# Optimization experiments

Measured on AMD Instinct MI355X. Metric: run time of the kernel, lower is better.

The kernel has to match this reference:

```python
import jax, jax.numpy as jnp
from jax import lax
import numpy as np

B, NQ, NT = 32, 256, 512
INF = jnp.float32(1e30)  # stand-in for float('inf') mask fill; all targets are valid here
W_TRANS, W_QPOS, W_ROT = 1.0, 1.0, 1.0


def setup_inputs() -> dict:
    key = jax.random.key(0)
    k1, k2, k3, k4 = jax.random.split(key, 4)
    rot = jax.random.normal(k3, (B, NQ, 4), jnp.float32)
    rot = rot / jnp.linalg.norm(rot, axis=-1, keepdims=True)  # unit quaternions
    return {
        "translation_norm": jax.random.normal(k1, (B, NQ, 3), jnp.float32),
        "qpos_norm": jax.random.normal(k2, (B, NQ, 16), jnp.float32),
        "rotation": rot,
        "norm_pose": jax.random.normal(k4, (B, NT, 23), jnp.float32),
    }


def _l1_cost(p, t):
    # p: [B, NQ, D], t: [B, NT, D] -> [B, NQ, NT] pairwise L1
    return jnp.abs(p[:, :, None, :] - t[:, None, :, :]).sum(-1)


def _final_cost(translation_norm, qpos_norm, rotation, norm_pose):
    valid = jnp.abs(norm_pose).sum(-1) > 0  # [B, NT]
    cost = (W_TRANS * _l1_cost(translation_norm, norm_pose[..., :3])
            + W_QPOS * _l1_cost(qpos_norm, norm_pose[..., 3:19])
            + W_ROT * (1.0 - jnp.abs(jnp.einsum('bqd,bnd->bqn', rotation, norm_pose[..., 19:]))))
    return jnp.where(valid[:, None, :], cost, INF)


def _hungarian(cost):
    """Rectangular LSAP via Jonker-Volgenant shortest augmenting path
    (same algorithm as scipy.optimize.linear_sum_assignment).
    cost: [n, m] with n <= m. Returns col4row [n]: matched column per row."""
    n, m = cost.shape

    def solve_row(carry, cur_row):
        u, v, col4row, row4col = carry

        # --- Dijkstra-like search for the shortest augmenting path ---
        def s_cond(st):
            return st[6] < 0  # until a free column (sink) is found

        def s_body(st):
            i, minVal, SR, SC, spc, path, _sink = st
            SR = SR.at[i].set(True)
            r = minVal + cost[i] - u[i] - v          # reduced costs for row i
            upd = (~SC) & (r < spc)
            spc = jnp.where(upd, r, spc)
            path = jnp.where(upd, i, path)
            masked = jnp.where(SC, INF, spc)
            j = jnp.argmin(masked).astype(jnp.int32)
            minVal = masked[j]
            SC = SC.at[j].set(True)
            free = row4col[j] < 0
            sink = jnp.where(free, j, jnp.int32(-1))
            i = jnp.where(free, i, row4col[j])
            return (i, minVal, SR, SC, spc, path, sink)

        st0 = (cur_row, jnp.float32(0.0),
               jnp.zeros((n,), bool), jnp.zeros((m,), bool),
               jnp.full((m,), INF), jnp.full((m,), -1, jnp.int32), jnp.int32(-1))
        _i, minVal, SR, SC, spc, path, sink = lax.while_loop(s_cond, s_body, st0)

        # --- dual variable updates ---
        spc_row = spc[jnp.clip(col4row, 0, m - 1)]  # [n]; invalid rows masked by SR
        du = jnp.where(jnp.arange(n) == cur_row, minVal, minVal - spc_row)
        u = u + jnp.where(SR, du, 0.0)
        v = v - jnp.where(SC, minVal - spc, 0.0)

        # --- augment along the alternating path back to cur_row ---
        def a_cond(st):
            return ~st[3]

        def a_body(st):
            j, c4r, r4c, _done = st
            i = path[j]
            r4c = r4c.at[j].set(i)
            nj = c4r[i]
            c4r = c4r.at[i].set(j)
            return (nj, c4r, r4c, i == cur_row)

        _, col4row, row4col, _ = lax.while_loop(
            a_cond, a_body, (sink, col4row, row4col, False))
        return (u, v, col4row, row4col), None

    carry0 = (jnp.zeros((n,), jnp.float32), jnp.zeros((m,), jnp.float32),
              jnp.full((n,), -1, jnp.int32), jnp.full((m,), -1, jnp.int32))
    (u, v, col4row, row4col), _ = lax.scan(
        solve_row, carry0, jnp.arange(n, dtype=jnp.int32))
    return col4row


def reference(translation_norm, qpos_norm, rotation, norm_pose):
    final_cost = _final_cost(translation_norm, qpos_norm, rotation, norm_pose)
    # batched Hungarian (replaces per-batch scipy linear_sum_assignment loop)
    per_query_gt_inds = jax.vmap(_hungarian)(final_cost)        # [B, NQ]
    query_matched_mask = jnp.ones_like(per_query_gt_inds)        # all matched (NT >= NQ)
    return final_cost, per_query_gt_inds, query_matched_mask
```

## Files before the change

### kernel.cpp

```cpp
#include <hip/hip_runtime.h>

constexpr int kB  = 32;
constexpr int kNQ = 256;
constexpr int kNT = 512;
constexpr float kInf = 1e30f;
constexpr int kQTile = 8;
constexpr int kSlots = 56;
constexpr int kStride = 544;

__global__ __launch_bounds__(512)
void cost_kernel(const float* __restrict__ trans,
                 const float* __restrict__ qpos,
                 const float* __restrict__ rot,
                 const float* __restrict__ pose,
                 float* __restrict__ cost)
{
    __shared__ float sPose[kNT * 23];

    const int b     = blockIdx.x;
    const int qBase = blockIdx.y * kQTile;
    const int tid   = threadIdx.x;

    const float* pb = pose + (size_t)b * kNT * 23;
    for (int idx = tid; idx < kNT * 23; idx += 512) sPose[idx] = pb[idx];
    __syncthreads();

    float T[23];
    #pragma unroll
    for (int d = 0; d < 23; ++d) T[d] = sPose[tid * 23 + d];

    float s = 0.f;
    #pragma unroll
    for (int d = 0; d < 23; ++d) s += fabsf(T[d]);
    const bool valid = (s > 0.f);

    const float* tr = trans + ((size_t)b * kNQ + qBase) * 3;
    const float* qp = qpos  + ((size_t)b * kNQ + qBase) * 16;
    const float* rt = rot   + ((size_t)b * kNQ + qBase) * 4;
    float* cb = cost + ((size_t)b * kNQ + qBase) * kNT + tid;

    #pragma unroll
    for (int q = 0; q < kQTile; ++q) {
        const float Q0 = tr[q * 3 + 0], Q1 = tr[q * 3 + 1], Q2 = tr[q * 3 + 2];
        float a = fabsf(Q0 - T[0]);
        a += fabsf(Q1 - T[1]);
        a += fabsf(Q2 - T[2]);
        float bsum = 0.f;
        #pragma unroll
        for (int d = 0; d < 16; ++d) bsum += fabsf(qp[q * 16 + d] - T[3 + d]);
        const float r0 = rt[q * 4 + 0], r1 = rt[q * 4 + 1];
        const float r2 = rt[q * 4 + 2], r3 = rt[q * 4 + 3];
        float dot = r0 * T[19] + r1 * T[20] + r2 * T[21] + r3 * T[22];
        float c = (a + bsum) + (1.0f - fabsf(dot));
        cb[(size_t)q * kNT] = valid ? c : kInf;
    }
}

__device__ __forceinline__ unsigned wave_min_u32(unsigned x) {
    unsigned t;
    t = (unsigned)__builtin_amdgcn_update_dpp((int)0xFFFFFFFF, (int)x, 0x111, 0xF, 0xF, false); x = t < x ? t : x;
    t = (unsigned)__builtin_amdgcn_update_dpp((int)0xFFFFFFFF, (int)x, 0x112, 0xF, 0xF, false); x = t < x ? t : x;
    t = (unsigned)__builtin_amdgcn_update_dpp((int)0xFFFFFFFF, (int)x, 0x114, 0xF, 0xF, false); x = t < x ? t : x;
    t = (unsigned)__builtin_amdgcn_update_dpp((int)0xFFFFFFFF, (int)x, 0x118, 0xF, 0xF, false); x = t < x ? t : x;
    t = (unsigned)__builtin_amdgcn_update_dpp((int)0xFFFFFFFF, (int)x, 0x142, 0xF, 0xF, false); x = t < x ? t : x;
    t = (unsigned)__builtin_amdgcn_update_dpp((int)0xFFFFFFFF, (int)x, 0x143, 0xF, 0xF, false); x = t < x ? t : x;
    return (unsigned)__builtin_amdgcn_readlane((int)x, 63);
}

__global__ __launch_bounds__(256)
void hungarian_kernel(const float* __restrict__ cost,
                      float* __restrict__ outInds,
                      float* __restrict__ outMask)
{
    __shared__ float rowCache[kSlots * kStride];
    __shared__ float u[kNQ];
    __shared__ int   col4row[kNQ];
    __shared__ int   row4col[kNT];
    __shared__ int   colBest[kNT];
    __shared__ int   pathL[kNT];
    __shared__ int   rowArg[kNQ];

    const int b   = blockIdx.x;
    const int tid = threadIdx.x;
    const float* __restrict__ C = cost + (size_t)b * kNQ * kNT;

    {
        const float4* Crow = (const float4*)(C + (size_t)tid * kNT);
        float bm = kInf; int barg = 0;
        #pragma unroll 4
        for (int j4 = 0; j4 < kNT / 4; ++j4) {
            float4 cc = Crow[j4];
            const int jb = j4 * 4;
            if (cc.x < bm) { bm = cc.x; barg = jb + 0; }
            if (cc.y < bm) { bm = cc.y; barg = jb + 1; }
            if (cc.z < bm) { bm = cc.z; barg = jb + 2; }
            if (cc.w < bm) { bm = cc.w; barg = jb + 3; }
        }
        u[tid]      = bm;
        rowArg[tid] = barg;
        col4row[tid] = -1;
    }
    row4col[tid] = -1;         row4col[tid + 256] = -1;
    colBest[tid] = 0x7fffffff; colBest[tid + 256] = 0x7fffffff;
    __syncthreads();
    atomicMin(&colBest[rowArg[tid]], tid);
    __syncthreads();
    {
        const int j = rowArg[tid];
        if (colBest[j] == tid) { col4row[tid] = j; row4col[j] = tid; }
    }
    __syncthreads();

    if (tid < 64) {
        const int lane = tid;
        const int laneOff = (lane >> 3) * 68 + (lane & 7) * 8;
        typedef float v2f __attribute__((ext_vector_type(2)));

        float vR[8];
        #pragma unroll
        for (int c = 0; c < 8; ++c) vR[c] = 0.f;

        int tagReg = -1;
        int rr     = 0;

        for (int cur = 0; cur < kNQ; ++cur) {
            if (col4row[cur] >= 0) continue;

            float spcR[8]; int pathR[8]; float mskA[8]; float frzV[8]; int frzP[8];
            #pragma unroll
            for (int c = 0; c < 8; ++c) {
                spcR[c] = kInf; pathR[c] = -1; mskA[c] = 0.f;
                frzV[c] = 0.f;  frzP[c] = -1;
            }
            unsigned scMask = 0;

            int   i      = cur;
            float minVal = 0.f;
            int   sink   = -1;

            for (int guard = 0; guard < kNT + 2 && sink < 0; ++guard) {
                const float ui = u[i];
                float4 p0, p1;
                const unsigned long long hm = __ballot(tagReg == i);
                if (hm != 0ull) {
                    const int slot = (int)__ffsll(hm) - 1;
                    const float4* lp = (const float4*)&rowCache[slot * kStride + laneOff];
                    p0 = lp[0]; p1 = lp[1];
                } else {
                    const float4* rp = (const float4*)(C + (size_t)i * kNT + lane * 8);
                    p0 = rp[0]; p1 = rp[1];
                    if (guard != 0) {
                        float4* wp = (float4*)&rowCache[rr * kStride + laneOff];
                        wp[0] = p0; wp[1] = p1;
                        if (lane == rr) tagReg = i;
                        rr = rr + 1; if (rr == kSlots) rr = 0;
                    }
                }

                const v2f cc2[4] = { {p0.x, p0.y}, {p0.z, p0.w},
                                     {p1.x, p1.y}, {p1.z, p1.w} };
                const v2f mv2 = { minVal, minVal };
                const v2f ui2 = { ui, ui };
                float r8[8];
                #pragma unroll
                for (int p = 0; p < 4; ++p) {
                    const v2f vv = { vR[2*p], vR[2*p + 1] };
                    const v2f rp2 = ((mv2 + cc2[p]) - ui2) - vv;
                    r8[2*p] = rp2.x; r8[2*p + 1] = rp2.y;
                }
                #pragma unroll
                for (int c = 0; c < 8; ++c) {
                    const bool lt = r8[c] < spcR[c];
                    spcR[c]  = lt ? r8[c] : spcR[c];
                    pathR[c] = lt ? i : pathR[c];
                }

                float mskv[8];
                #pragma unroll
                for (int p = 0; p < 4; ++p) {
                    const v2f s2 = { spcR[2*p], spcR[2*p + 1] };
                    const v2f a2 = { mskA[2*p], mskA[2*p + 1] };
                    const v2f m2 = s2 + a2;
                    mskv[2*p] = m2.x; mskv[2*p + 1] = m2.y;
                }
                unsigned sp[8];
                #pragma unroll
                for (int c = 0; c < 8; ++c) sp[c] = __float_as_uint(mskv[c]);
                unsigned mA = sp[1] < sp[0] ? sp[1] : sp[0]; int aA = sp[1] < sp[0] ? 1 : 0;
                unsigned mB = sp[3] < sp[2] ? sp[3] : sp[2]; int aB = sp[3] < sp[2] ? 3 : 2;
                unsigned mC = sp[5] < sp[4] ? sp[5] : sp[4]; int aC = sp[5] < sp[4] ? 5 : 4;
                unsigned mD = sp[7] < sp[6] ? sp[7] : sp[6]; int aD = sp[7] < sp[6] ? 7 : 6;
                unsigned mAB = mB < mA ? mB : mA; int aAB = mB < mA ? aB : aA;
                unsigned mCD = mD < mC ? mD : mC; int aCD = mD < mC ? aD : aC;
                unsigned lvu = mCD < mAB ? mCD : mAB; int lc = mCD < mAB ? aCD : aAB;
                const int lix  = lane * 8 + lc;
                const int spec = row4col[lix];

                const unsigned gmu = wave_min_u32(lvu);
                const unsigned long long bal = __ballot(lvu == gmu);
                const int wl    = (int)__ffsll(bal) - 1;
                const int jstar = __builtin_amdgcn_readlane(lix, wl);
                const int own   = __builtin_amdgcn_readlane(spec, wl);
                minVal = __uint_as_float(gmu);

                if (own < 0) sink = jstar;
                else         i    = own;

                if (wl == lane) {
                    const int lcw = jstar & 7;
                    scMask |= 1u << lcw;
                    #pragma unroll
                    for (int c = 0; c < 8; ++c) {
                        if (c == lcw) {
                            mskA[c] = __builtin_inff();
                            frzV[c] = minVal;
                            frzP[c] = pathR[c];
                        }
                    }
                }
            }

            if (lane == 0) u[cur] += minVal;
            #pragma unroll
            for (int c = 0; c < 8; ++c) {
                if ((scMask >> c) & 1u) {
                    const int j = lane * 8 + c;
                    const int r = row4col[j];
                    const float d = minVal - frzV[c];
                    if (r >= 0) u[r] += d;
                    vR[c] -= d;
                    pathL[j] = frzP[c];
                }
            }
            __threadfence_block();

            if (lane == 0 && sink >= 0) {
                int j = sink;
                while (true) {
                    const int pi = pathL[j];
                    row4col[j] = pi;
                    const int nj = col4row[pi];
                    col4row[pi] = j;
                    if (pi == cur) break;
                    j = nj;
                }
            }
            __threadfence_block();
        }
    }
    __syncthreads();

    outInds[(size_t)b * kNQ + tid] = (float)col4row[tid];
    outMask[(size_t)b * kNQ + tid] = 1.0f;
}

extern "C" void kernel_launch(void* const* d_in, const int* in_sizes, int n_in,
                              void* d_out, int out_size, void* d_ws, size_t ws_size,
                              hipStream_t stream) {
    const float* trans = (const float*)d_in[0];
    const float* qpos  = (const float*)d_in[1];
    const float* rot   = (const float*)d_in[2];
    const float* pose  = (const float*)d_in[3];

    float* out  = (float*)d_out;
    float* cost = out;
    float* inds = out + (size_t)kB * kNQ * kNT;
    float* mask = inds + (size_t)kB * kNQ;

    dim3 g1(kB, kNQ / kQTile);
    cost_kernel<<<g1, 512, 0, stream>>>(trans, qpos, rot, pose, cost);
    hungarian_kernel<<<kB, 256, 0, stream>>>(cost, inds, mask);
}
```

Baseline: 429.2 us.

## Add auction-style augmenting row reduction before shortest-path Hungarian phase

Adds a Jonker-Volgenant augmenting row reduction pass that runs before the shortest augmenting path loop. A wave-wide top-two minimum reduction assigns each free row to its best reduced-cost column, lowers that column's price by the gap to the second minimum, and pushes any displaced owner back onto a free list. The aim is to leave fewer unassigned rows for the expensive Dijkstra-style searches. The pass is capped at a fixed step count, and tie handling or a degenerate zero gap could leave the dual variables less tight than before.

```diff
diff --git a/kernel.cpp b/kernel.cpp
--- a/kernel.cpp
+++ b/kernel.cpp
@@ -7,6 +7,8 @@
 constexpr int kQTile = 8;
 constexpr int kSlots = 56;
 constexpr int kStride = 544;
+constexpr int kArrCap = 768;
+constexpr int kListCap = 1024;
 
 __global__ __launch_bounds__(512)
 void cost_kernel(const float* __restrict__ trans,
@@ -67,6 +69,24 @@
     return (unsigned)__builtin_amdgcn_readlane((int)x, 63);
 }
 
+__device__ __forceinline__ void wave_min2_f32(float &m1, float &m2) {
+#define MIN2_STEP(CTRL)                                                          \
+    {                                                                            \
+        const float o1 = __int_as_float(__builtin_amdgcn_update_dpp(             \
+            0x7F800000, __float_as_int(m1), CTRL, 0xF, 0xF, false));             \
+        const float o2 = __int_as_float(__builtin_amdgcn_update_dpp(             \
+            0x7F800000, __float_as_int(m2), CTRL, 0xF, 0xF, false));             \
+        const bool  lt  = o1 < m1;                                               \
+        const float n2a = fminf(m2, o1);                                         \
+        const float n2b = fminf(o2, m1);                                         \
+        m2 = lt ? n2b : n2a;                                                     \
+        m1 = lt ? o1 : m1;                                                       \
+    }
+    MIN2_STEP(0x111) MIN2_STEP(0x112) MIN2_STEP(0x114)
+    MIN2_STEP(0x118) MIN2_STEP(0x142) MIN2_STEP(0x143)
+#undef MIN2_STEP
+}
+
 __global__ __launch_bounds__(256)
 void hungarian_kernel(const float* __restrict__ cost,
                       float* __restrict__ outInds,
@@ -79,6 +99,8 @@
     __shared__ int   colBest[kNT];
     __shared__ int   pathL[kNT];
     __shared__ int   rowArg[kNQ];
+    __shared__ int   freeL[kListCap];
+    __shared__ int   flCnt;
 
     const int b   = blockIdx.x;
     const int tid = threadIdx.x;
@@ -122,6 +144,101 @@
 
         int tagReg = -1;
         int rr     = 0;
+
+        if (lane == 0) flCnt = 0;
+        #pragma unroll
+        for (int e = 0; e < 4; ++e) {
+            const int r = lane * 4 + e;
+            if (col4row[r] < 0) { const int t = atomicAdd(&flCnt, 1); freeL[t] = r; }
+        }
+        __threadfence_block();
+
+        {
+            int head = 0;
+            for (int steps = 0; steps < kArrCap; ++steps) {
+                const int tail = flCnt;
+                if (head >= tail) break;
+                const int i = freeL[head]; ++head;
+                if (col4row[i] >= 0) continue;
+
+                const unsigned long long hm = __ballot(tagReg == i);
+                float4 p0, p1;
+                if (hm != 0ull) {
+                    const int slot = (int)__ffsll(hm) - 1;
+                    const float4* lp = (const float4*)&rowCache[slot * kStride + laneOff];
+                    p0 = lp[0]; p1 = lp[1];
+                } else {
+                    const float4* rp = (const float4*)(C + (size_t)i * kNT + lane * 8);
+                    p0 = rp[0]; p1 = rp[1];
+                    float4* wp = (float4*)&rowCache[rr * kStride + laneOff];
+                    wp[0] = p0; wp[1] = p1;
+                    if (lane == rr) tagReg = i;
+                    rr = rr + 1; if (rr == kSlots) rr = 0;
+                }
+
+                const float vals[8] = { p0.x, p0.y, p0.z, p0.w,
+                                        p1.x, p1.y, p1.z, p1.w };
+                float rc8[8];
+                #pragma unroll
+                for (int c = 0; c < 8; ++c) rc8[c] = vals[c] - vR[c];
+
+                float lm1, lm2; int lc;
+                {
+                    float a1[4], a2[4]; int ai[4];
+                    #pragma unroll
+                    for (int p = 0; p < 4; ++p) {
+                        const float x = rc8[2 * p], y = rc8[2 * p + 1];
+                        const bool sw = y < x;
+                        a1[p] = sw ? y : x;
+                        a2[p] = sw ? x : y;
+                        ai[p] = sw ? 2 * p + 1 : 2 * p;
+                    }
+                    float b1A, b2A; int biA;
+                    { const bool lt = a1[1] < a1[0];
+                      b2A = lt ? fminf(a2[1], a1[0]) : fminf(a2[0], a1[1]);
+                      b1A = lt ? a1[1] : a1[0];
+                      biA = lt ? ai[1] : ai[0]; }
+                    float b1B, b2B; int biB;
+                    { const bool lt = a1[3] < a1[2];
+                      b2B = lt ? fminf(a2[3], a1[2]) : fminf(a2[2], a1[3]);
+                      b1B = lt ? a1[3] : a1[2];
+                      biB = lt ? ai[3] : ai[2]; }
+                    { const bool lt = b1B < b1A;
+                      lm2 = lt ? fminf(b2B, b1A) : fminf(b2A, b1B);
+                      lm1 = lt ? b1B : b1A;
+                      lc  = lt ? biB : biA; }
+                }
+                const int spec = row4col[lane * 8 + lc];
+
+                float w1 = lm1, w2 = lm2;
+                wave_min2_f32(w1, w2);
+                const float g1 = __int_as_float(__builtin_amdgcn_readlane(__float_as_int(w1), 63));
+                const float g2 = __int_as_float(__builtin_amdgcn_readlane(__float_as_int(w2), 63));
+
+                const unsigned long long bal = __ballot(lm1 == g1);
+                const int wl  = (int)__ffsll(bal) - 1;
+                const int j1  = __builtin_amdgcn_readlane(lane * 8 + lc, wl);
+                const int own = __builtin_amdgcn_readlane(spec, wl);
+
+                if (wl == lane) {
+                    const int lcw = j1 & 7;
+                    const float d = g2 - g1;
+                    #pragma unroll
+                    for (int c = 0; c < 8; ++c) if (c == lcw) vR[c] -= d;
+                }
+                if (lane == 0) {
+                    u[i] = g2;
+                    row4col[j1] = i;
+                    col4row[i]  = j1;
+                    if (own >= 0) {
+                        col4row[own] = -1;
+                        const int t = flCnt;
+                        if (t < kListCap) { freeL[t] = own; flCnt = t + 1; }
+                    }
+                }
+                __threadfence_block();
+            }
+        }
 
         for (int cur = 0; cur < kNQ; ++cur) {
             if (col4row[cur] >= 0) continue;
```

Result: slower. 500.0 us (+16.5%).
